# Kernel tuning notes

Hardware: AMD Instinct MI355X
Metric: run time of the kernel (lower is better)

## Reference

```python
import jax, jax.numpy as jnp
import numpy as np

N_NODES = 50000
N_GROUPS = 512
D_FEAT = 128
D_HID = 128
N_CLASS = 16
NEG_SLOPE = 0.2


def gat_conv(x, edge_index, W, a_src, a_dst, bias, n):
    """Single-head PyG-style GATConv (with self-loops, eval mode / no dropout)."""
    h = x @ W  # [n, D_HID]
    loop = jnp.arange(n)
    src = jnp.concatenate([edge_index[0], loop])  # neighbors j
    dst = jnp.concatenate([edge_index[1], loop])  # targets i
    a_s = h @ a_src  # [n]
    a_d = h @ a_dst  # [n]
    e = jax.nn.leaky_relu(a_s[src] + a_d[dst], NEG_SLOPE)  # [E+n]
    # segment softmax over incoming edges of each dst node
    m = jax.ops.segment_max(e, dst, num_segments=n)
    e = jnp.exp(e - m[dst])
    denom = jax.ops.segment_sum(e, dst, num_segments=n)
    alpha = e / denom[dst]
    out = jax.ops.segment_sum(alpha[:, None] * h[src], dst, num_segments=n)
    return out + bias


def setup_inputs() -> dict:
    key = jax.random.key(0)
    ks = jax.random.split(key, 12)
    s_f = 1.0 / np.sqrt(D_FEAT)
    s_h = 1.0 / np.sqrt(D_HID)
    return {
        "x_full": jax.random.normal(ks[0], (N_NODES, D_FEAT), jnp.float32),
        "x_group": jax.random.normal(ks[1], (N_GROUPS, D_FEAT), jnp.float32),
        "W_full": jax.random.normal(ks[2], (D_FEAT, D_HID), jnp.float32) * s_f,
        "a_src_full": jax.random.normal(ks[3], (D_HID,), jnp.float32) * s_h,
        "a_dst_full": jax.random.normal(ks[4], (D_HID,), jnp.float32) * s_h,
        "bias_full": jnp.zeros((D_HID,), jnp.float32),
        "W_group": jax.random.normal(ks[5], (D_FEAT, D_HID), jnp.float32) * s_f,
        "a_src_group": jax.random.normal(ks[6], (D_HID,), jnp.float32) * s_h,
        "a_dst_group": jax.random.normal(ks[7], (D_HID,), jnp.float32) * s_h,
        "bias_group": jnp.zeros((D_HID,), jnp.float32),
        "fc_W": jax.random.normal(ks[8], (D_HID, N_CLASS), jnp.float32) * s_h,
        "fc_b": jnp.zeros((N_CLASS,), jnp.float32),
        "edge_index_full": jax.random.randint(ks[9], (2, 600000), 0, N_NODES, jnp.int64),
        "edge_index_group": jax.random.randint(ks[10], (2, 4096), 0, N_GROUPS, jnp.int64),
        "node_group": jax.random.randint(ks[11], (N_NODES,), 0, N_GROUPS, jnp.int64),
    }


def reference(x_full, x_group, W_full, a_src_full, a_dst_full, bias_full,
              W_group, a_src_group, a_dst_group, bias_group, fc_W, fc_b,
              edge_index_full, edge_index_group, node_group):
    full_x = jax.nn.elu(gat_conv(x_full, edge_index_full, W_full, a_src_full,
                                 a_dst_full, bias_full, N_NODES))   # [N, D_HID]
    group_x = jax.nn.elu(gat_conv(x_group, edge_index_group, W_group, a_src_group,
                                  a_dst_group, bias_group, N_GROUPS))  # [G, D_HID]

    # mean feature of groups adjacent to each group (edges src->dst in group graph)
    gsrc, gdst = edge_index_group[0], edge_index_group[1]
    adj_sum = jax.ops.segment_sum(group_x[gdst], gsrc, num_segments=N_GROUPS)
    cnt = jax.ops.segment_sum(jnp.ones_like(gsrc, jnp.float32), gsrc, num_segments=N_GROUPS)
    adj_mean = adj_sum / jnp.maximum(cnt, 1.0)[:, None]  # [G, D_HID]

    gf = group_x[node_group]   # group feature per node, [N, D_HID]
    am = adj_mean[node_group]  # adjacent-group mean per node, [N, D_HID]

    # dot(node, group_feature) and mean_j dot(node, adj_j) == dot(node, adj_mean)
    iw_group = jnp.sum(full_x * gf, axis=-1, keepdims=True)  # [N, 1]
    iw_adj = jnp.sum(full_x * am, axis=-1, keepdims=True)    # [N, 1]

    updated = full_x + iw_group * gf + iw_adj * am  # [N, D_HID]
    out = updated @ fc_W + fc_b                     # [N, N_CLASS]
    return (out, updated)
```

## Files before the change

kernel.cpp:

```cpp
#include <hip/hip_runtime.h>

typedef unsigned short u16;
typedef unsigned int u32;

static __device__ __forceinline__ float lrelu(float x) { return x >= 0.f ? x : 0.2f * x; }

static __device__ __forceinline__ u16 f2bf(float f) {
    u32 u = __float_as_uint(f);
    u += 0x7FFF + ((u >> 16) & 1);
    return (u16)(u >> 16);
}
static __device__ __forceinline__ float bf2f(u16 h) {
    return __uint_as_float((u32)h << 16);
}

__global__ __launch_bounds__(256) void gemm_both_kernel(
        const float* __restrict__ Xf, const float* __restrict__ Wf,
        const float* __restrict__ asf, const float* __restrict__ adf,
        u16* __restrict__ Hbf, float* __restrict__ as_f, float* __restrict__ ad_f, int N,
        const float* __restrict__ Xg, const float* __restrict__ Wg,
        const float* __restrict__ asg, const float* __restrict__ adg,
        u16* __restrict__ Hbg, float* __restrict__ as_g, float* __restrict__ ad_g, int G,
        int nbFull) {
    const float* X; const float* W; const float* av; const float* dv;
    u16* Hb; float* as_out; float* ad_out; int n_lim; long base;
    if (blockIdx.x < nbFull) {
        X = Xf; W = Wf; av = asf; dv = adf; Hb = Hbf; as_out = as_f; ad_out = ad_f;
        n_lim = N; base = (long)blockIdx.x * 32;
    } else {
        X = Xg; W = Wg; av = asg; dv = adg; Hb = Hbg; as_out = as_g; ad_out = ad_g;
        n_lim = G; base = (long)(blockIdx.x - nbFull) * 32;
    }
    __shared__ float Ws[64 * 128];
    __shared__ float Xs[32 * 128];
    int tid = threadIdx.x;
    float4* Ws4 = (float4*)Ws;
    float4* Xs4 = (float4*)Xs;
    const float4* X4 = (const float4*)(X + base * 128);
    for (int i = tid; i < 1024; i += 256) {
        int r = i >> 5;
        Xs4[i] = (base + r < n_lim) ? X4[i] : make_float4(0.f, 0.f, 0.f, 0.f);
    }
    int fgrp = tid & 31;
    int n0 = (tid >> 5) * 4;
    float4 acc[4] = {};
    for (int half = 0; half < 2; ++half) {
        __syncthreads();
        const float4* W4 = (const float4*)(W + half * 64 * 128);
        for (int i = tid; i < 2048; i += 256) Ws4[i] = W4[i];
        __syncthreads();
        #pragma unroll 4
        for (int kk = 0; kk < 64; ++kk) {
            float4 w = Ws4[kk * 32 + fgrp];
            #pragma unroll
            for (int j = 0; j < 4; ++j) {
                float x = Xs[(n0 + j) * 128 + half * 64 + kk];
                acc[j].x += x * w.x; acc[j].y += x * w.y;
                acc[j].z += x * w.z; acc[j].w += x * w.w;
            }
        }
    }
    float4 as4 = ((const float4*)av)[fgrp];
    float4 ad4 = ((const float4*)dv)[fgrp];
    float ps[4], pd[4];
    #pragma unroll
    for (int j = 0; j < 4; ++j) {
        ps[j] = acc[j].x * as4.x + acc[j].y * as4.y + acc[j].z * as4.z + acc[j].w * as4.w;
        pd[j] = acc[j].x * ad4.x + acc[j].y * ad4.y + acc[j].z * ad4.z + acc[j].w * ad4.w;
    }
    #pragma unroll
    for (int off = 16; off; off >>= 1) {
        #pragma unroll
        for (int j = 0; j < 4; ++j) {
            ps[j] += __shfl_xor(ps[j], off);
            pd[j] += __shfl_xor(pd[j], off);
        }
    }
    if ((tid & 31) == 0) {
        #pragma unroll
        for (int j = 0; j < 4; ++j) {
            long n = base + n0 + j;
            if (n < n_lim) { as_out[n] = ps[j]; ad_out[n] = pd[j]; }
        }
    }
    #pragma unroll
    for (int j = 0; j < 4; ++j) {
        long n = base + n0 + j;
        if (n < n_lim) {
            ushort4 hv;
            hv.x = f2bf(acc[j].x); hv.y = f2bf(acc[j].y);
            hv.z = f2bf(acc[j].z); hv.w = f2bf(acc[j].w);
            ((ushort4*)(Hb + n * 128))[fgrp] = hv;
        }
    }
}

__global__ __launch_bounds__(256) void hist2_kernel(const int* __restrict__ efd, int E, int N,
                                                    const int* __restrict__ egd, int Eg, int G,
                                                    int Npad, int* __restrict__ deg) {
    int i = blockIdx.x * 256 + threadIdx.x;
    int totF = E + N;
    int tot = totF + Eg + G;
    if (i >= tot) return;
    int d;
    if (i < E) d = efd[i];
    else if (i < totF) d = i - E;
    else {
        int j = i - totF;
        d = Npad + ((j < Eg) ? egd[j] : (j - Eg));
    }
    atomicAdd(&deg[d], 1);
}

__global__ __launch_bounds__(256) void scan1_kernel(const int* __restrict__ deg, int n,
                                                    int* __restrict__ bsum) {
    __shared__ int s[256];
    int i = blockIdx.x * 256 + threadIdx.x;
    s[threadIdx.x] = (i < n) ? deg[i] : 0;
    __syncthreads();
    for (int off = 128; off; off >>= 1) {
        if (threadIdx.x < off) s[threadIdx.x] += s[threadIdx.x + off];
        __syncthreads();
    }
    if (threadIdx.x == 0) bsum[blockIdx.x] = s[0];
}

__global__ __launch_bounds__(256) void scan3_kernel(int* __restrict__ deg, int n, int nb,
                                                    const int* __restrict__ bsum,
                                                    int* __restrict__ offs, int Ltot) {
    __shared__ int sb[256];
    __shared__ int s[256];
    int t = threadIdx.x;
    sb[t] = (t < nb) ? bsum[t] : 0;
    __syncthreads();
    for (int off = 1; off < 256; off <<= 1) {
        int u = (t >= off) ? sb[t - off] : 0;
        __syncthreads();
        sb[t] += u;
        __syncthreads();
    }
    int blockOff = (blockIdx.x == 0) ? 0 : sb[blockIdx.x - 1];
    if (blockIdx.x == 0 && t == 0) offs[Ltot] = sb[nb - 1];

    int i = blockIdx.x * 256 + t;
    int v = (i < n) ? deg[i] : 0;
    s[t] = v;
    __syncthreads();
    for (int off = 1; off < 256; off <<= 1) {
        int u = (t >= off) ? s[t - off] : 0;
        __syncthreads();
        s[t] += u;
        __syncthreads();
    }
    if (i < n) {
        int excl = s[t] - v + blockOff;
        offs[i] = excl;
        deg[i] = excl;
    }
}

__global__ __launch_bounds__(256) void place2_kernel(const int* __restrict__ efs,
                                                     const int* __restrict__ efd, int E, int N,
                                                     const int* __restrict__ egs,
                                                     const int* __restrict__ egd, int Eg, int G,
                                                     int Npad,
                                                     const float* __restrict__ a_s,
                                                     const float* __restrict__ a_d,
                                                     const float* __restrict__ a_sg,
                                                     const float* __restrict__ a_dg,
                                                     int* __restrict__ cursor,
                                                     int* __restrict__ slot,
                                                     float* __restrict__ eslot) {
    int i = blockIdx.x * 256 + threadIdx.x;
    int totF = E + N;
    int tot = totF + Eg + G;
    if (i >= tot) return;
    int s, d, dcur;
    float av;
    if (i < totF) {
        if (i < E) { s = efs[i]; d = efd[i]; } else { s = d = i - E; }
        av = a_s[s] + a_d[d];
        dcur = d;
    } else {
        int j = i - totF;
        if (j < Eg) { s = egs[j]; d = egd[j]; } else { s = d = j - Eg; }
        av = a_sg[s] + a_dg[d];
        dcur = Npad + d;
    }
    float e = expf(lrelu(av));
    int pos = atomicAdd(&cursor[dcur], 1);
    slot[pos] = s;
    eslot[pos] = e;
}

__global__ __launch_bounds__(256) void pull2_kernel(const u16* __restrict__ Hf,
                                                    const u16* __restrict__ Hg,
                                                    const int* __restrict__ offs,
                                                    const int* __restrict__ slot,
                                                    const float* __restrict__ eslot,
                                                    const float* __restrict__ bias_f,
                                                    const float* __restrict__ bias_g,
                                                    float* __restrict__ fx,
                                                    float* __restrict__ gx,
                                                    int N, int G, int Npad) {
    int gid = blockIdx.x * 256 + threadIdx.x;
    int w = gid >> 6, lane = gid & 63;
    const u16* H;
    const float* bias;
    float* out;
    int idx;
    if (w < N) {
        H = Hf; bias = bias_f; out = fx + (long)w * 128; idx = w;
    } else if (w < N + G) {
        int g = w - N;
        H = Hg; bias = bias_g; out = gx + (long)g * 128; idx = Npad + g;
    } else return;
    int beg = offs[idx], end = offs[idx + 1];
    float accx = 0.f, accy = 0.f, ssum = 0.f;
    int k = beg;
    for (; k + 2 <= end; k += 2) {
        int s0 = slot[k], s1 = slot[k + 1];
        float e0 = eslot[k], e1 = eslot[k + 1];
        ushort2 h0 = ((const ushort2*)H)[(long)s0 * 64 + lane];
        ushort2 h1 = ((const ushort2*)H)[(long)s1 * 64 + lane];
        accx += e0 * bf2f(h0.x) + e1 * bf2f(h1.x);
        accy += e0 * bf2f(h0.y) + e1 * bf2f(h1.y);
        ssum += e0 + e1;
    }
    if (k < end) {
        int s0 = slot[k];
        float e0 = eslot[k];
        ushort2 h0 = ((const ushort2*)H)[(long)s0 * 64 + lane];
        accx += e0 * bf2f(h0.x);
        accy += e0 * bf2f(h0.y);
        ssum += e0;
    }
    float inv = 1.f / ssum;
    float2 b = ((const float2*)bias)[lane];
    float ox = accx * inv + b.x;
    float oy = accy * inv + b.y;
    ox = ox > 0.f ? ox : expm1f(ox);
    oy = oy > 0.f ? oy : expm1f(oy);
    ((float2*)out)[lane] = make_float2(ox, oy);
}

__global__ __launch_bounds__(256) void adj_kernel(const int* __restrict__ gsrc,
                                                  const int* __restrict__ gdst, int Eg,
                                                  const float* __restrict__ gx,
                                                  float* __restrict__ adj_sum,
                                                  float* __restrict__ cnt) {
    int gid = blockIdx.x * 256 + threadIdx.x;
    int i = gid >> 6, lane = gid & 63;
    if (i >= Eg) return;
    int s = gsrc[i], d = gdst[i];
    float2 gv = ((const float2*)gx)[(long)d * 64 + lane];
    atomicAdd(&adj_sum[(long)s * 128 + 2 * lane], gv.x);
    atomicAdd(&adj_sum[(long)s * 128 + 2 * lane + 1], gv.y);
    if (lane == 0) atomicAdd(&cnt[s], 1.f);
}

__global__ __launch_bounds__(256) void final_kernel(const int* __restrict__ node_group,
                                                    const float* __restrict__ gx,
                                                    const float* __restrict__ adj_sum,
                                                    const float* __restrict__ cnt,
                                                    const float* __restrict__ fcW,
                                                    const float* __restrict__ fcb,
                                                    float* __restrict__ upd,
                                                    float* __restrict__ out, int N) {
    int gid = blockIdx.x * 256 + threadIdx.x;
    int n = gid >> 6, lane = gid & 63;
    if (n >= N) return;
    int g = node_group[n];
    float2 row = ((const float2*)upd)[(long)n * 64 + lane];
    float2 gf = ((const float2*)gx)[(long)g * 64 + lane];
    float inv_cnt = 1.f / fmaxf(cnt[g], 1.f);
    float2 amv = ((const float2*)adj_sum)[(long)g * 64 + lane];
    float amx = amv.x * inv_cnt, amy = amv.y * inv_cnt;
    float pg = row.x * gf.x + row.y * gf.y;
    float pa = row.x * amx + row.y * amy;
    #pragma unroll
    for (int off = 32; off; off >>= 1) {
        pg += __shfl_xor(pg, off);
        pa += __shfl_xor(pa, off);
    }
    float ux = row.x + pg * gf.x + pa * amx;
    float uy = row.y + pg * gf.y + pa * amy;
    ((float2*)upd)[(long)n * 64 + lane] = make_float2(ux, uy);

    float v[16];
    const float4* fW4 = (const float4*)fcW;
    #pragma unroll
    for (int q = 0; q < 4; ++q) {
        float4 w0 = fW4[(2 * lane) * 4 + q];
        float4 w1 = fW4[(2 * lane + 1) * 4 + q];
        v[4 * q + 0] = ux * w0.x + uy * w1.x;
        v[4 * q + 1] = ux * w0.y + uy * w1.y;
        v[4 * q + 2] = ux * w0.z + uy * w1.z;
        v[4 * q + 3] = ux * w0.w + uy * w1.w;
    }
    #pragma unroll
    for (int stage = 0; stage < 4; ++stage) {
        int width = 32 >> stage;
        int half = 8 >> stage;
        bool hi = (lane & width) != 0;
        #pragma unroll
        for (int c = 0; c < half; ++c) {
            float send = hi ? v[c] : v[c + half];
            float recv = __shfl_xor(send, width);
            float keep = hi ? v[c + half] : v[c];
            v[c] = keep + recv;
        }
    }
    v[0] += __shfl_xor(v[0], 1);
    v[0] += __shfl_xor(v[0], 2);
    int cls = (lane >> 2) & 15;
    if ((lane & 3) == 0) out[(long)n * 16 + cls] = v[0] + fcb[cls];
}

extern "C" void kernel_launch(void* const* d_in, const int* in_sizes, int n_in,
                              void* d_out, int out_size, void* d_ws, size_t ws_size,
                              hipStream_t stream) {
    const float* x_full = (const float*)d_in[0];
    const float* x_group = (const float*)d_in[1];
    const float* W_full = (const float*)d_in[2];
    const float* a_src_full = (const float*)d_in[3];
    const float* a_dst_full = (const float*)d_in[4];
    const float* bias_full = (const float*)d_in[5];
    const float* W_group = (const float*)d_in[6];
    const float* a_src_g = (const float*)d_in[7];
    const float* a_dst_g = (const float*)d_in[8];
    const float* bias_g = (const float*)d_in[9];
    const float* fc_W = (const float*)d_in[10];
    const float* fc_b = (const float*)d_in[11];
    const int* ef = (const int*)d_in[12];
    const int* eg = (const int*)d_in[13];
    const int* node_group = (const int*)d_in[14];

    int N = in_sizes[0] / 128;
    int G = in_sizes[1] / 128;
    int E = in_sizes[12] / 2;
    int Eg = in_sizes[13] / 2;
    const int* ef_src = ef;
    const int* ef_dst = ef + E;
    const int* eg_src = eg;
    const int* eg_dst = eg + Eg;

    int Npad = (N + 255) & ~255;
    int Ltot = Npad + G;
    int LtotPad = (Ltot + 255) & ~255;
    int totF = E + N;
    int tot = totF + Eg + G;

    float* out_cls = (float*)d_out;
    float* fx = out_cls + (long)N * 16;

    char* w = (char*)d_ws;
    auto alloc = [&](size_t bytes) {
        char* p = w;
        w += (bytes + 255) & ~(size_t)255;
        return p;
    };
    u16* h_full = (u16*)alloc((size_t)N * 128 * 2);
    u16* h_g = (u16*)alloc((size_t)G * 128 * 2);
    float* a_s = (float*)alloc((size_t)N * 4);
    float* a_d = (float*)alloc((size_t)N * 4);
    float* a_sg = (float*)alloc((size_t)G * 4);
    float* a_dg = (float*)alloc((size_t)G * 4);
    float* gx = (float*)alloc((size_t)G * 128 * 4);
    float* adj_sum = (float*)alloc((size_t)G * 128 * 4);
    float* cnt = (float*)alloc((size_t)G * 4);
    int* deg = (int*)alloc((size_t)LtotPad * 4);
    int* offs = (int*)alloc((size_t)(LtotPad + 1) * 4);
    int* slot = (int*)alloc((size_t)tot * 4);
    float* eslot = (float*)alloc((size_t)tot * 4);
    int* bsum = (int*)alloc(256 * 4);

    size_t zero_span = (char*)(deg + LtotPad) - (char*)adj_sum;
    (void)hipMemsetAsync(adj_sum, 0, zero_span, stream);

    auto cdiv = [](int a, int b) { return (a + b - 1) / b; };

    int nbFull = cdiv(N, 32);
    gemm_both_kernel<<<nbFull + cdiv(G, 32), 256, 0, stream>>>(
        x_full, W_full, a_src_full, a_dst_full, h_full, a_s, a_d, N,
        x_group, W_group, a_src_g, a_dst_g, h_g, a_sg, a_dg, G, nbFull);

    int nb = cdiv(Ltot, 256);
    hist2_kernel<<<cdiv(tot, 256), 256, 0, stream>>>(ef_dst, E, N, eg_dst, Eg, G, Npad, deg);
    scan1_kernel<<<nb, 256, 0, stream>>>(deg, Ltot, bsum);
    scan3_kernel<<<nb, 256, 0, stream>>>(deg, Ltot, nb, bsum, offs, Ltot);
    place2_kernel<<<cdiv(tot, 256), 256, 0, stream>>>(ef_src, ef_dst, E, N, eg_src, eg_dst,
                                                      Eg, G, Npad, a_s, a_d, a_sg, a_dg,
                                                      deg, slot, eslot);

    pull2_kernel<<<cdiv((N + G) * 64, 256), 256, 0, stream>>>(h_full, h_g, offs, slot, eslot,
                                                              bias_full, bias_g, fx, gx,
                                                              N, G, Npad);

    adj_kernel<<<cdiv(Eg * 64, 256), 256, 0, stream>>>(eg_src, eg_dst, Eg, gx, adj_sum, cnt);
    final_kernel<<<cdiv(N * 64, 256), 256, 0, stream>>>(node_group, gx, adj_sum, cnt, fc_W,
                                                        fc_b, fx, out_cls, N);
}
```

Baseline: 337.7 us.

## Split final FC by linearity into per-node and per-group projections

Uses linearity of the classifier: out = full_x·W + pg·(gf·W) + pa·(am·W) + b. The full_x projection moves into the pull kernel's epilogue, and a new small kernel computes the per-group projections of group features and adjacent means. The final kernel then combines a few scalars per class instead of running the 16-wide shuffle reduction on every node. This adds a kernel launch, an N×16 intermediate buffer, and extra work and register pressure in the pull kernel.

```diff
diff --git a/kernel.cpp b/kernel.cpp
--- a/kernel.cpp
+++ b/kernel.cpp
@@ -12,6 +12,61 @@
 }
 static __device__ __forceinline__ float bf2f(u16 h) {
     return __uint_as_float((u32)h << 16);
+}
+
+static __device__ __forceinline__ float fc_reduce16(float f0, float f1, int lane,
+                                                    const float4* __restrict__ fW4) {
+    float4 w00 = fW4[(2 * lane) * 4 + 0], w01 = fW4[(2 * lane) * 4 + 1];
+    float4 w02 = fW4[(2 * lane) * 4 + 2], w03 = fW4[(2 * lane) * 4 + 3];
+    float4 w10 = fW4[(2 * lane + 1) * 4 + 0], w11 = fW4[(2 * lane + 1) * 4 + 1];
+    float4 w12 = fW4[(2 * lane + 1) * 4 + 2], w13 = fW4[(2 * lane + 1) * 4 + 3];
+    float4 q0, q1, q2, q3;
+    q0.x = f0 * w00.x + f1 * w10.x; q0.y = f0 * w00.y + f1 * w10.y;
+    q0.z = f0 * w00.z + f1 * w10.z; q0.w = f0 * w00.w + f1 * w10.w;
+    q1.x = f0 * w01.x + f1 * w11.x; q1.y = f0 * w01.y + f1 * w11.y;
+    q1.z = f0 * w01.z + f1 * w11.z; q1.w = f0 * w01.w + f1 * w11.w;
+    q2.x = f0 * w02.x + f1 * w12.x; q2.y = f0 * w02.y + f1 * w12.y;
+    q2.z = f0 * w02.z + f1 * w12.z; q2.w = f0 * w02.w + f1 * w12.w;
+    q3.x = f0 * w03.x + f1 * w13.x; q3.y = f0 * w03.y + f1 * w13.y;
+    q3.z = f0 * w03.z + f1 * w13.z; q3.w = f0 * w03.w + f1 * w13.w;
+    bool h5 = (lane & 32) != 0, h4 = (lane & 16) != 0;
+    bool h3 = (lane & 8) != 0, h2 = (lane & 4) != 0;
+    float4 s0, s1, k0, k1;
+    s0.x = h5 ? q0.x : q2.x; s0.y = h5 ? q0.y : q2.y;
+    s0.z = h5 ? q0.z : q2.z; s0.w = h5 ? q0.w : q2.w;
+    s1.x = h5 ? q1.x : q3.x; s1.y = h5 ? q1.y : q3.y;
+    s1.z = h5 ? q1.z : q3.z; s1.w = h5 ? q1.w : q3.w;
+    s0.x = __shfl_xor(s0.x, 32); s0.y = __shfl_xor(s0.y, 32);
+    s0.z = __shfl_xor(s0.z, 32); s0.w = __shfl_xor(s0.w, 32);
+    s1.x = __shfl_xor(s1.x, 32); s1.y = __shfl_xor(s1.y, 32);
+    s1.z = __shfl_xor(s1.z, 32); s1.w = __shfl_xor(s1.w, 32);
+    k0.x = h5 ? q2.x : q0.x; k0.y = h5 ? q2.y : q0.y;
+    k0.z = h5 ? q2.z : q0.z; k0.w = h5 ? q2.w : q0.w;
+    k1.x = h5 ? q3.x : q1.x; k1.y = h5 ? q3.y : q1.y;
+    k1.z = h5 ? q3.z : q1.z; k1.w = h5 ? q3.w : q1.w;
+    float4 a0, a1;
+    a0.x = k0.x + s0.x; a0.y = k0.y + s0.y; a0.z = k0.z + s0.z; a0.w = k0.w + s0.w;
+    a1.x = k1.x + s1.x; a1.y = k1.y + s1.y; a1.z = k1.z + s1.z; a1.w = k1.w + s1.w;
+    float4 sB, kB;
+    sB.x = h4 ? a0.x : a1.x; sB.y = h4 ? a0.y : a1.y;
+    sB.z = h4 ? a0.z : a1.z; sB.w = h4 ? a0.w : a1.w;
+    sB.x = __shfl_xor(sB.x, 16); sB.y = __shfl_xor(sB.y, 16);
+    sB.z = __shfl_xor(sB.z, 16); sB.w = __shfl_xor(sB.w, 16);
+    kB.x = h4 ? a1.x : a0.x; kB.y = h4 ? a1.y : a0.y;
+    kB.z = h4 ? a1.z : a0.z; kB.w = h4 ? a1.w : a0.w;
+    float4 b;
+    b.x = kB.x + sB.x; b.y = kB.y + sB.y; b.z = kB.z + sB.z; b.w = kB.w + sB.w;
+    float sCx = h3 ? b.x : b.z, sCy = h3 ? b.y : b.w;
+    sCx = __shfl_xor(sCx, 8); sCy = __shfl_xor(sCy, 8);
+    float kCx = h3 ? b.z : b.x, kCy = h3 ? b.w : b.y;
+    float c2x = kCx + sCx, c2y = kCy + sCy;
+    float sD = h2 ? c2x : c2y;
+    sD = __shfl_xor(sD, 4);
+    float kD = h2 ? c2y : c2x;
+    float r = kD + sD;
+    r += __shfl_xor(r, 1);
+    r += __shfl_xor(r, 2);
+    return r;
 }
 
 __global__ __launch_bounds__(256) void gemm_both_kernel(
@@ -200,8 +255,10 @@
                                                     const float* __restrict__ eslot,
                                                     const float* __restrict__ bias_f,
                                                     const float* __restrict__ bias_g,
+                                                    const float* __restrict__ fcW,
                                                     float* __restrict__ fx,
                                                     float* __restrict__ gx,
+                                                    float* __restrict__ fxW,
                                                     int N, int G, int Npad) {
     int gid = blockIdx.x * 256 + threadIdx.x;
     int w = gid >> 6, lane = gid & 63;
@@ -209,7 +266,8 @@
     const float* bias;
     float* out;
     int idx;
-    if (w < N) {
+    bool isFull = (w < N);
+    if (isFull) {
         H = Hf; bias = bias_f; out = fx + (long)w * 128; idx = w;
     } else if (w < N + G) {
         int g = w - N;
@@ -242,6 +300,11 @@
     ox = ox > 0.f ? ox : expm1f(ox);
     oy = oy > 0.f ? oy : expm1f(oy);
     ((float2*)out)[lane] = make_float2(ox, oy);
+    if (isFull) {
+        float r = fc_reduce16(ox, oy, lane, (const float4*)fcW);
+        int cls = (lane >> 2) & 15;
+        if ((lane & 3) == 0) fxW[(long)w * 16 + cls] = r;
+    }
 }
 
 __global__ __launch_bounds__(256) void adj_kernel(const int* __restrict__ gsrc,
@@ -259,62 +322,61 @@
     if (lane == 0) atomicAdd(&cnt[s], 1.f);
 }
 
-__global__ __launch_bounds__(256) void final_kernel(const int* __restrict__ node_group,
-                                                    const float* __restrict__ gx,
-                                                    const float* __restrict__ adj_sum,
-                                                    const float* __restrict__ cnt,
-                                                    const float* __restrict__ fcW,
-                                                    const float* __restrict__ fcb,
-                                                    float* __restrict__ upd,
-                                                    float* __restrict__ out, int N) {
+__global__ __launch_bounds__(256) void groupfc_kernel(const float* __restrict__ gx,
+                                                      const float* __restrict__ adj_sum,
+                                                      const float* __restrict__ cnt,
+                                                      const float* __restrict__ fcW,
+                                                      float* __restrict__ adj_mean,
+                                                      float* __restrict__ gfW,
+                                                      float* __restrict__ amW, int G) {
+    int gid = blockIdx.x * 256 + threadIdx.x;
+    int g = gid >> 6, lane = gid & 63;
+    if (g >= G) return;
+    float inv = 1.f / fmaxf(cnt[g], 1.f);
+    float2 as2 = ((const float2*)adj_sum)[(long)g * 64 + lane];
+    float2 am = make_float2(as2.x * inv, as2.y * inv);
+    ((float2*)adj_mean)[(long)g * 64 + lane] = am;
+    float2 gf = ((const float2*)gx)[(long)g * 64 + lane];
+    const float4* fW4 = (const float4*)fcW;
+    float rg = fc_reduce16(gf.x, gf.y, lane, fW4);
+    float ra = fc_reduce16(am.x, am.y, lane, fW4);
+    int cls = (lane >> 2) & 15;
+    if ((lane & 3) == 0) {
+        gfW[(long)g * 16 + cls] = rg;
+        amW[(long)g * 16 + cls] = ra;
+    }
+}
+
+__global__ __launch_bounds__(256) void final3_kernel(const int* __restrict__ node_group,
+                                                     const float* __restrict__ gx,
+                                                     const float* __restrict__ adj_mean,
+                                                     const float* __restrict__ gfW,
+                                                     const float* __restrict__ amW,
+                                                     const float* __restrict__ fxW,
+                                                     const float* __restrict__ fcb,
+                                                     float* __restrict__ upd,
+                                                     float* __restrict__ out, int N) {
     int gid = blockIdx.x * 256 + threadIdx.x;
     int n = gid >> 6, lane = gid & 63;
     if (n >= N) return;
     int g = node_group[n];
     float2 row = ((const float2*)upd)[(long)n * 64 + lane];
     float2 gf = ((const float2*)gx)[(long)g * 64 + lane];
-    float inv_cnt = 1.f / fmaxf(cnt[g], 1.f);
-    float2 amv = ((const float2*)adj_sum)[(long)g * 64 + lane];
-    float amx = amv.x * inv_cnt, amy = amv.y * inv_cnt;
+    float2 am = ((const float2*)adj_mean)[(long)g * 64 + lane];
     float pg = row.x * gf.x + row.y * gf.y;
-    float pa = row.x * amx + row.y * amy;
+    float pa = row.x * am.x + row.y * am.y;
     #pragma unroll
     for (int off = 32; off; off >>= 1) {
         pg += __shfl_xor(pg, off);
         pa += __shfl_xor(pa, off);
     }
-    float ux = row.x + pg * gf.x + pa * amx;
-    float uy = row.y + pg * gf.y + pa * amy;
+    float ux = row.x + pg * gf.x + pa * am.x;
+    float uy = row.y + pg * gf.y + pa * am.y;
     ((float2*)upd)[(long)n * 64 + lane] = make_float2(ux, uy);
-
-    float v[16];
-    const float4* fW4 = (const float4*)fcW;
-    #pragma unroll
-    for (int q = 0; q < 4; ++q) {
-        float4 w0 = fW4[(2 * lane) * 4 + q];
-        float4 w1 = fW4[(2 * lane + 1) * 4 + q];
-        v[4 * q + 0] = ux * w0.x + uy * w1.x;
-        v[4 * q + 1] = ux * w0.y + uy * w1.y;
-        v[4 * q + 2] = ux * w0.z + uy * w1.z;
-        v[4 * q + 3] = ux * w0.w + uy * w1.w;
-    }
-    #pragma unroll
-    for (int stage = 0; stage < 4; ++stage) {
-        int width = 32 >> stage;
-        int half = 8 >> stage;
-        bool hi = (lane & width) != 0;
-        #pragma unroll
-        for (int c = 0; c < half; ++c) {
-            float send = hi ? v[c] : v[c + half];
-            float recv = __shfl_xor(send, width);
-            float keep = hi ? v[c + half] : v[c];
-            v[c] = keep + recv;
-        }
-    }
-    v[0] += __shfl_xor(v[0], 1);
-    v[0] += __shfl_xor(v[0], 2);
-    int cls = (lane >> 2) & 15;
-    if ((lane & 3) == 0) out[(long)n * 16 + cls] = v[0] + fcb[cls];
+    if (lane < 16) {
+        out[(long)n * 16 + lane] = fxW[(long)n * 16 + lane] + pg * gfW[(long)g * 16 + lane] +
+                                   pa * amW[(long)g * 16 + lane] + fcb[lane];
+    }
 }
 
 extern "C" void kernel_launch(void* const* d_in, const int* in_sizes, int n_in,
@@ -367,6 +429,10 @@
     float* a_sg = (float*)alloc((size_t)G * 4);
     float* a_dg = (float*)alloc((size_t)G * 4);
     float* gx = (float*)alloc((size_t)G * 128 * 4);
+    float* adj_mean = (float*)alloc((size_t)G * 128 * 4);
+    float* fxW = (float*)alloc((size_t)N * 16 * 4);
+    float* gfW = (float*)alloc((size_t)G * 16 * 4);
+    float* amW = (float*)alloc((size_t)G * 16 * 4);
     float* adj_sum = (float*)alloc((size_t)G * 128 * 4);
     float* cnt = (float*)alloc((size_t)G * 4);
     int* deg = (int*)alloc((size_t)LtotPad * 4);
@@ -394,10 +460,12 @@
                                                       deg, slot, eslot);
 
     pull2_kernel<<<cdiv((N + G) * 64, 256), 256, 0, stream>>>(h_full, h_g, offs, slot, eslot,
-                                                              bias_full, bias_g, fx, gx,
-                                                              N, G, Npad);
+                                                              bias_full, bias_g, fc_W,
+                                                              fx, gx, fxW, N, G, Npad);
 
     adj_kernel<<<cdiv(Eg * 64, 256), 256, 0, stream>>>(eg_src, eg_dst, Eg, gx, adj_sum, cnt);
-    final_kernel<<<cdiv(N * 64, 256), 256, 0, stream>>>(node_group, gx, adj_sum, cnt, fc_W,
-                                                        fc_b, fx, out_cls, N);
-}
+    groupfc_kernel<<<cdiv(G * 64, 256), 256, 0, stream>>>(gx, adj_sum, cnt, fc_W,
+                                                          adj_mean, gfW, amW, G);
+    final3_kernel<<<cdiv(N * 64, 256), 256, 0, stream>>>(node_group, gx, adj_mean, gfW, amW,
+                                                         fxW, fc_b, fx, out_cls, N);
+}
```

Result: faster. 315.4 us (-6.6%).

## Fuse full-graph aggregation into final kernel, pack edge slots, widen gather loads

Applied to the files above, without the earlier changes.

Merges the degree histogram into the GEMM launch and splits the pull kernel. The group-graph aggregation now runs on its own first, and the full-graph aggregation is fused with the final interaction and classifier kernel, so the full_x intermediate is never written and re-read. Source index and edge weight are packed into one int2 array. The gather loads edge metadata cooperatively and broadcasts it with shuffles, with each wave processing four edges at once using 16-byte bf16 row loads. This adds register pressure and shuffle reductions, and wave utilisation drops for low-degree nodes because lanes are split into four sub-groups.

```diff
diff --git a/kernel.cpp b/kernel.cpp
--- a/kernel.cpp
+++ b/kernel.cpp
@@ -10,18 +10,37 @@
     u += 0x7FFF + ((u >> 16) & 1);
     return (u16)(u >> 16);
 }
-static __device__ __forceinline__ float bf2f(u16 h) {
-    return __uint_as_float((u32)h << 16);
-}
-
-__global__ __launch_bounds__(256) void gemm_both_kernel(
+static __device__ __forceinline__ float bflo(u32 u) { return __uint_as_float(u << 16); }
+static __device__ __forceinline__ float bfhi(u32 u) { return __uint_as_float(u & 0xffff0000u); }
+
+__global__ __launch_bounds__(256) void gemm_hist_kernel(
         const float* __restrict__ Xf, const float* __restrict__ Wf,
         const float* __restrict__ asf, const float* __restrict__ adf,
         u16* __restrict__ Hbf, float* __restrict__ as_f, float* __restrict__ ad_f, int N,
         const float* __restrict__ Xg, const float* __restrict__ Wg,
         const float* __restrict__ asg, const float* __restrict__ adg,
         u16* __restrict__ Hbg, float* __restrict__ as_g, float* __restrict__ ad_g, int G,
-        int nbFull) {
+        int nbFull, int nbGemm,
+        const int* __restrict__ efd, int E, const int* __restrict__ egd, int Eg,
+        int Npad, int* __restrict__ deg) {
+    __shared__ float Ws[64 * 128];
+    __shared__ float Xs[32 * 128];
+    int tid = threadIdx.x;
+    if (blockIdx.x >= nbGemm) {
+        int i = (blockIdx.x - nbGemm) * 256 + tid;
+        int totF = E + N;
+        int tot = totF + Eg + G;
+        if (i >= tot) return;
+        int d;
+        if (i < E) d = efd[i];
+        else if (i < totF) d = i - E;
+        else {
+            int j = i - totF;
+            d = Npad + ((j < Eg) ? egd[j] : (j - Eg));
+        }
+        atomicAdd(&deg[d], 1);
+        return;
+    }
     const float* X; const float* W; const float* av; const float* dv;
     u16* Hb; float* as_out; float* ad_out; int n_lim; long base;
     if (blockIdx.x < nbFull) {
@@ -31,9 +50,6 @@
         X = Xg; W = Wg; av = asg; dv = adg; Hb = Hbg; as_out = as_g; ad_out = ad_g;
         n_lim = G; base = (long)(blockIdx.x - nbFull) * 32;
     }
-    __shared__ float Ws[64 * 128];
-    __shared__ float Xs[32 * 128];
-    int tid = threadIdx.x;
     float4* Ws4 = (float4*)Ws;
     float4* Xs4 = (float4*)Xs;
     const float4* X4 = (const float4*)(X + base * 128);
@@ -95,23 +111,6 @@
     }
 }
 
-__global__ __launch_bounds__(256) void hist2_kernel(const int* __restrict__ efd, int E, int N,
-                                                    const int* __restrict__ egd, int Eg, int G,
-                                                    int Npad, int* __restrict__ deg) {
-    int i = blockIdx.x * 256 + threadIdx.x;
-    int totF = E + N;
-    int tot = totF + Eg + G;
-    if (i >= tot) return;
-    int d;
-    if (i < E) d = efd[i];
-    else if (i < totF) d = i - E;
-    else {
-        int j = i - totF;
-        d = Npad + ((j < Eg) ? egd[j] : (j - Eg));
-    }
-    atomicAdd(&deg[d], 1);
-}
-
 __global__ __launch_bounds__(256) void scan1_kernel(const int* __restrict__ deg, int n,
                                                     int* __restrict__ bsum) {
     __shared__ int s[256];
@@ -169,8 +168,7 @@
                                                      const float* __restrict__ a_sg,
                                                      const float* __restrict__ a_dg,
                                                      int* __restrict__ cursor,
-                                                     int* __restrict__ slot,
-                                                     float* __restrict__ eslot) {
+                                                     int2* __restrict__ sepack) {
     int i = blockIdx.x * 256 + threadIdx.x;
     int totF = E + N;
     int tot = totF + Eg + G;
@@ -189,59 +187,121 @@
     }
     float e = expf(lrelu(av));
     int pos = atomicAdd(&cursor[dcur], 1);
-    slot[pos] = s;
-    eslot[pos] = e;
-}
-
-__global__ __launch_bounds__(256) void pull2_kernel(const u16* __restrict__ Hf,
-                                                    const u16* __restrict__ Hg,
-                                                    const int* __restrict__ offs,
-                                                    const int* __restrict__ slot,
-                                                    const float* __restrict__ eslot,
-                                                    const float* __restrict__ bias_f,
-                                                    const float* __restrict__ bias_g,
-                                                    float* __restrict__ fx,
-                                                    float* __restrict__ gx,
-                                                    int N, int G, int Npad) {
+    sepack[pos] = make_int2(s, __float_as_int(e));
+}
+
+#define PULL_GATHER_BODY(H16, beg, end)                                          \
+    for (int b = (beg); b < (end); b += 64) {                                    \
+        int m = (end) - b;                                                       \
+        if (m > 64) m = 64;                                                      \
+        int2 se = (lane < m) ? sepack[b + lane] : make_int2(0, 0);               \
+        int sl = se.x;                                                           \
+        float el = __int_as_float(se.y);                                         \
+        int kend = (m + 3) & ~3;                                                 \
+        int k = 0;                                                               \
+        for (; k + 16 <= kend; k += 16) {                                        \
+            int s0 = __shfl(sl, k + sub);                                        \
+            float e0 = __shfl(el, k + sub);                                      \
+            int s1 = __shfl(sl, k + 4 + sub);                                    \
+            float e1 = __shfl(el, k + 4 + sub);                                  \
+            int s2 = __shfl(sl, k + 8 + sub);                                    \
+            float e2 = __shfl(el, k + 8 + sub);                                  \
+            int s3 = __shfl(sl, k + 12 + sub);                                   \
+            float e3 = __shfl(el, k + 12 + sub);                                 \
+            uint4 h0 = H16[(long)s0 * 16 + fc];                                  \
+            uint4 h1 = H16[(long)s1 * 16 + fc];                                  \
+            uint4 h2 = H16[(long)s2 * 16 + fc];                                  \
+            uint4 h3 = H16[(long)s3 * 16 + fc];                                  \
+            a0 += e0 * bflo(h0.x); a1 += e0 * bfhi(h0.x);                        \
+            a2 += e0 * bflo(h0.y); a3 += e0 * bfhi(h0.y);                        \
+            a4 += e0 * bflo(h0.z); a5 += e0 * bfhi(h0.z);                        \
+            a6 += e0 * bflo(h0.w); a7 += e0 * bfhi(h0.w);                        \
+            a0 += e1 * bflo(h1.x); a1 += e1 * bfhi(h1.x);                        \
+            a2 += e1 * bflo(h1.y); a3 += e1 * bfhi(h1.y);                        \
+            a4 += e1 * bflo(h1.z); a5 += e1 * bfhi(h1.z);                        \
+            a6 += e1 * bflo(h1.w); a7 += e1 * bfhi(h1.w);                        \
+            a0 += e2 * bflo(h2.x); a1 += e2 * bfhi(h2.x);                        \
+            a2 += e2 * bflo(h2.y); a3 += e2 * bfhi(h2.y);                        \
+            a4 += e2 * bflo(h2.z); a5 += e2 * bfhi(h2.z);                        \
+            a6 += e2 * bflo(h2.w); a7 += e2 * bfhi(h2.w);                        \
+            a0 += e3 * bflo(h3.x); a1 += e3 * bfhi(h3.x);                        \
+            a2 += e3 * bflo(h3.y); a3 += e3 * bfhi(h3.y);                        \
+            a4 += e3 * bflo(h3.z); a5 += e3 * bfhi(h3.z);                        \
+            a6 += e3 * bflo(h3.w); a7 += e3 * bfhi(h3.w);                        \
+            ss += (e0 + e1) + (e2 + e3);                                         \
+        }                                                                        \
+        for (; k + 8 <= kend; k += 8) {                                          \
+            int s0 = __shfl(sl, k + sub);                                        \
+            float e0 = __shfl(el, k + sub);                                      \
+            int s1 = __shfl(sl, k + 4 + sub);                                    \
+            float e1 = __shfl(el, k + 4 + sub);                                  \
+            uint4 h0 = H16[(long)s0 * 16 + fc];                                  \
+            uint4 h1 = H16[(long)s1 * 16 + fc];                                  \
+            a0 += e0 * bflo(h0.x); a1 += e0 * bfhi(h0.x);                        \
+            a2 += e0 * bflo(h0.y); a3 += e0 * bfhi(h0.y);                        \
+            a4 += e0 * bflo(h0.z); a5 += e0 * bfhi(h0.z);                        \
+            a6 += e0 * bflo(h0.w); a7 += e0 * bfhi(h0.w);                        \
+            a0 += e1 * bflo(h1.x); a1 += e1 * bfhi(h1.x);                        \
+            a2 += e1 * bflo(h1.y); a3 += e1 * bfhi(h1.y);                        \
+            a4 += e1 * bflo(h1.z); a5 += e1 * bfhi(h1.z);                        \
+            a6 += e1 * bflo(h1.w); a7 += e1 * bfhi(h1.w);                        \
+            ss += e0 + e1;                                                       \
+        }                                                                        \
+        if (k < kend) {                                                          \
+            int s0 = __shfl(sl, k + sub);                                        \
+            float e0 = __shfl(el, k + sub);                                      \
+            uint4 h0 = H16[(long)s0 * 16 + fc];                                  \
+            a0 += e0 * bflo(h0.x); a1 += e0 * bfhi(h0.x);                        \
+            a2 += e0 * bflo(h0.y); a3 += e0 * bfhi(h0.y);                        \
+            a4 += e0 * bflo(h0.z); a5 += e0 * bfhi(h0.z);                        \
+            a6 += e0 * bflo(h0.w); a7 += e0 * bfhi(h0.w);                        \
+            ss += e0;                                                            \
+        }                                                                        \
+    }                                                                            \
+    a0 += __shfl_xor(a0, 16); a0 += __shfl_xor(a0, 32);                          \
+    a1 += __shfl_xor(a1, 16); a1 += __shfl_xor(a1, 32);                          \
+    a2 += __shfl_xor(a2, 16); a2 += __shfl_xor(a2, 32);                          \
+    a3 += __shfl_xor(a3, 16); a3 += __shfl_xor(a3, 32);                          \
+    a4 += __shfl_xor(a4, 16); a4 += __shfl_xor(a4, 32);                          \
+    a5 += __shfl_xor(a5, 16); a5 += __shfl_xor(a5, 32);                          \
+    a6 += __shfl_xor(a6, 16); a6 += __shfl_xor(a6, 32);                          \
+    a7 += __shfl_xor(a7, 16); a7 += __shfl_xor(a7, 32);                          \
+    ss += __shfl_xor(ss, 16); ss += __shfl_xor(ss, 32);
+
+__global__ __launch_bounds__(256) void pull_g_kernel(const u16* __restrict__ Hg,
+                                                     const int* __restrict__ offs,
+                                                     const int2* __restrict__ sepack,
+                                                     const float* __restrict__ bias_g,
+                                                     float* __restrict__ gx,
+                                                     int G, int Npad) {
     int gid = blockIdx.x * 256 + threadIdx.x;
     int w = gid >> 6, lane = gid & 63;
-    const u16* H;
-    const float* bias;
-    float* out;
-    int idx;
-    if (w < N) {
-        H = Hf; bias = bias_f; out = fx + (long)w * 128; idx = w;
-    } else if (w < N + G) {
-        int g = w - N;
-        H = Hg; bias = bias_g; out = gx + (long)g * 128; idx = Npad + g;
-    } else return;
+    if (w >= G) return;
+    int idx = Npad + w;
     int beg = offs[idx], end = offs[idx + 1];
-    float accx = 0.f, accy = 0.f, ssum = 0.f;
-    int k = beg;
-    for (; k + 2 <= end; k += 2) {
-        int s0 = slot[k], s1 = slot[k + 1];
-        float e0 = eslot[k], e1 = eslot[k + 1];
-        ushort2 h0 = ((const ushort2*)H)[(long)s0 * 64 + lane];
-        ushort2 h1 = ((const ushort2*)H)[(long)s1 * 64 + lane];
-        accx += e0 * bf2f(h0.x) + e1 * bf2f(h1.x);
-        accy += e0 * bf2f(h0.y) + e1 * bf2f(h1.y);
-        ssum += e0 + e1;
-    }
-    if (k < end) {
-        int s0 = slot[k];
-        float e0 = eslot[k];
-        ushort2 h0 = ((const ushort2*)H)[(long)s0 * 64 + lane];
-        accx += e0 * bf2f(h0.x);
-        accy += e0 * bf2f(h0.y);
-        ssum += e0;
-    }
-    float inv = 1.f / ssum;
-    float2 b = ((const float2*)bias)[lane];
-    float ox = accx * inv + b.x;
-    float oy = accy * inv + b.y;
-    ox = ox > 0.f ? ox : expm1f(ox);
-    oy = oy > 0.f ? oy : expm1f(oy);
-    ((float2*)out)[lane] = make_float2(ox, oy);
+    const uint4* H16 = (const uint4*)Hg;
+    int sub = lane >> 4;
+    int fc = lane & 15;
+    float a0 = 0.f, a1 = 0.f, a2 = 0.f, a3 = 0.f;
+    float a4 = 0.f, a5 = 0.f, a6 = 0.f, a7 = 0.f;
+    float ss = 0.f;
+    PULL_GATHER_BODY(H16, beg, end)
+    if (sub == 0) {
+        float inv = 1.f / ss;
+        const float4* b4 = (const float4*)bias_g;
+        float4 bA = b4[fc * 2], bB = b4[fc * 2 + 1];
+        float o0 = a0 * inv + bA.x, o1 = a1 * inv + bA.y;
+        float o2 = a2 * inv + bA.z, o3 = a3 * inv + bA.w;
+        float o4 = a4 * inv + bB.x, o5 = a5 * inv + bB.y;
+        float o6 = a6 * inv + bB.z, o7 = a7 * inv + bB.w;
+        o0 = o0 > 0.f ? o0 : expm1f(o0); o1 = o1 > 0.f ? o1 : expm1f(o1);
+        o2 = o2 > 0.f ? o2 : expm1f(o2); o3 = o3 > 0.f ? o3 : expm1f(o3);
+        o4 = o4 > 0.f ? o4 : expm1f(o4); o5 = o5 > 0.f ? o5 : expm1f(o5);
+        o6 = o6 > 0.f ? o6 : expm1f(o6); o7 = o7 > 0.f ? o7 : expm1f(o7);
+        float4* o4p = (float4*)(gx + (long)w * 128);
+        o4p[fc * 2] = make_float4(o0, o1, o2, o3);
+        o4p[fc * 2 + 1] = make_float4(o4, o5, o6, o7);
+    }
 }
 
 __global__ __launch_bounds__(256) void adj_kernel(const int* __restrict__ gsrc,
@@ -259,62 +319,96 @@
     if (lane == 0) atomicAdd(&cnt[s], 1.f);
 }
 
-__global__ __launch_bounds__(256) void final_kernel(const int* __restrict__ node_group,
-                                                    const float* __restrict__ gx,
-                                                    const float* __restrict__ adj_sum,
-                                                    const float* __restrict__ cnt,
-                                                    const float* __restrict__ fcW,
-                                                    const float* __restrict__ fcb,
-                                                    float* __restrict__ upd,
-                                                    float* __restrict__ out, int N) {
+__global__ __launch_bounds__(256) void pull_f_final_kernel(
+        const u16* __restrict__ Hf,
+        const int* __restrict__ offs,
+        const int2* __restrict__ sepack,
+        const float* __restrict__ bias_f,
+        const int* __restrict__ node_group,
+        const float* __restrict__ gx,
+        const float* __restrict__ adj_sum,
+        const float* __restrict__ cnt,
+        const float* __restrict__ fcW,
+        const float* __restrict__ fcb,
+        float* __restrict__ upd,
+        float* __restrict__ out, int N) {
     int gid = blockIdx.x * 256 + threadIdx.x;
-    int n = gid >> 6, lane = gid & 63;
-    if (n >= N) return;
-    int g = node_group[n];
-    float2 row = ((const float2*)upd)[(long)n * 64 + lane];
-    float2 gf = ((const float2*)gx)[(long)g * 64 + lane];
+    int w = gid >> 6, lane = gid & 63;
+    if (w >= N) return;
+    int beg = offs[w], end = offs[w + 1];
+    const uint4* H16 = (const uint4*)Hf;
+    int sub = lane >> 4;
+    int fc = lane & 15;
+    float a0 = 0.f, a1 = 0.f, a2 = 0.f, a3 = 0.f;
+    float a4 = 0.f, a5 = 0.f, a6 = 0.f, a7 = 0.f;
+    float ss = 0.f;
+    PULL_GATHER_BODY(H16, beg, end)
+    float inv = 1.f / ss;
+    const float4* b4 = (const float4*)bias_f;
+    float4 bA = b4[fc * 2], bB = b4[fc * 2 + 1];
+    float o0 = a0 * inv + bA.x, o1 = a1 * inv + bA.y;
+    float o2 = a2 * inv + bA.z, o3 = a3 * inv + bA.w;
+    float o4 = a4 * inv + bB.x, o5 = a5 * inv + bB.y;
+    float o6 = a6 * inv + bB.z, o7 = a7 * inv + bB.w;
+    o0 = o0 > 0.f ? o0 : expm1f(o0); o1 = o1 > 0.f ? o1 : expm1f(o1);
+    o2 = o2 > 0.f ? o2 : expm1f(o2); o3 = o3 > 0.f ? o3 : expm1f(o3);
+    o4 = o4 > 0.f ? o4 : expm1f(o4); o5 = o5 > 0.f ? o5 : expm1f(o5);
+    o6 = o6 > 0.f ? o6 : expm1f(o6); o7 = o7 > 0.f ? o7 : expm1f(o7);
+    int g = node_group[w];
+    const float4* gx4 = (const float4*)(gx + (long)g * 128);
+    const float4* am4 = (const float4*)(adj_sum + (long)g * 128);
     float inv_cnt = 1.f / fmaxf(cnt[g], 1.f);
-    float2 amv = ((const float2*)adj_sum)[(long)g * 64 + lane];
-    float amx = amv.x * inv_cnt, amy = amv.y * inv_cnt;
-    float pg = row.x * gf.x + row.y * gf.y;
-    float pa = row.x * amx + row.y * amy;
+    float4 gfA = gx4[fc * 2], gfB = gx4[fc * 2 + 1];
+    float4 amA = am4[fc * 2], amB = am4[fc * 2 + 1];
+    amA.x *= inv_cnt; amA.y *= inv_cnt; amA.z *= inv_cnt; amA.w *= inv_cnt;
+    amB.x *= inv_cnt; amB.y *= inv_cnt; amB.z *= inv_cnt; amB.w *= inv_cnt;
+    float pg = o0 * gfA.x + o1 * gfA.y + o2 * gfA.z + o3 * gfA.w +
+               o4 * gfB.x + o5 * gfB.y + o6 * gfB.z + o7 * gfB.w;
+    float pa = o0 * amA.x + o1 * amA.y + o2 * amA.z + o3 * amA.w +
+               o4 * amB.x + o5 * amB.y + o6 * amB.z + o7 * amB.w;
     #pragma unroll
-    for (int off = 32; off; off >>= 1) {
-        pg += __shfl_xor(pg, off);
-        pa += __shfl_xor(pa, off);
-    }
-    float ux = row.x + pg * gf.x + pa * amx;
-    float uy = row.y + pg * gf.y + pa * amy;
-    ((float2*)upd)[(long)n * 64 + lane] = make_float2(ux, uy);
-
-    float v[16];
+    for (int mask = 8; mask; mask >>= 1) {
+        pg += __shfl_xor(pg, mask);
+        pa += __shfl_xor(pa, mask);
+    }
+    float u0 = o0 + pg * gfA.x + pa * amA.x;
+    float u1 = o1 + pg * gfA.y + pa * amA.y;
+    float u2 = o2 + pg * gfA.z + pa * amA.z;
+    float u3 = o3 + pg * gfA.w + pa * amA.w;
+    float u4 = o4 + pg * gfB.x + pa * amB.x;
+    float u5 = o5 + pg * gfB.y + pa * amB.y;
+    float u6 = o6 + pg * gfB.z + pa * amB.z;
+    float u7 = o7 + pg * gfB.w + pa * amB.w;
+    if (sub == 0) {
+        float4* o4p = (float4*)(upd + (long)w * 128);
+        o4p[fc * 2] = make_float4(u0, u1, u2, u3);
+        o4p[fc * 2 + 1] = make_float4(u4, u5, u6, u7);
+    }
     const float4* fW4 = (const float4*)fcW;
+    int rb = (8 * fc) * 4 + sub;
+    float4 w0 = fW4[rb], w1 = fW4[rb + 4], w2 = fW4[rb + 8], w3 = fW4[rb + 12];
+    float4 w4 = fW4[rb + 16], w5 = fW4[rb + 20], w6 = fW4[rb + 24], w7 = fW4[rb + 28];
+    float4 p;
+    p.x = u0 * w0.x + u1 * w1.x + u2 * w2.x + u3 * w3.x +
+          u4 * w4.x + u5 * w5.x + u6 * w6.x + u7 * w7.x;
+    p.y = u0 * w0.y + u1 * w1.y + u2 * w2.y + u3 * w3.y +
+          u4 * w4.y + u5 * w5.y + u6 * w6.y + u7 * w7.y;
+    p.z = u0 * w0.z + u1 * w1.z + u2 * w2.z + u3 * w3.z +
+          u4 * w4.z + u5 * w5.z + u6 * w6.z + u7 * w7.z;
+    p.w = u0 * w0.w + u1 * w1.w + u2 * w2.w + u3 * w3.w +
+          u4 * w4.w + u5 * w5.w + u6 * w6.w + u7 * w7.w;
     #pragma unroll
-    for (int q = 0; q < 4; ++q) {
-        float4 w0 = fW4[(2 * lane) * 4 + q];
-        float4 w1 = fW4[(2 * lane + 1) * 4 + q];
-        v[4 * q + 0] = ux * w0.x + uy * w1.x;
-        v[4 * q + 1] = ux * w0.y + uy * w1.y;
-        v[4 * q + 2] = ux * w0.z + uy * w1.z;
-        v[4 * q + 3] = ux * w0.w + uy * w1.w;
-    }
-    #pragma unroll
-    for (int stage = 0; stage < 4; ++stage) {
-        int width = 32 >> stage;
-        int half = 8 >> stage;
-        bool hi = (lane & width) != 0;
-        #pragma unroll
-        for (int c = 0; c < half; ++c) {
-            float send = hi ? v[c] : v[c + half];
-            float recv = __shfl_xor(send, width);
-            float keep = hi ? v[c + half] : v[c];
-            v[c] = keep + recv;
-        }
-    }
-    v[0] += __shfl_xor(v[0], 1);
-    v[0] += __shfl_xor(v[0], 2);
-    int cls = (lane >> 2) & 15;
-    if ((lane & 3) == 0) out[(long)n * 16 + cls] = v[0] + fcb[cls];
+    for (int mask = 8; mask; mask >>= 1) {
+        p.x += __shfl_xor(p.x, mask);
+        p.y += __shfl_xor(p.y, mask);
+        p.z += __shfl_xor(p.z, mask);
+        p.w += __shfl_xor(p.w, mask);
+    }
+    if (fc == 0) {
+        float4 bb = ((const float4*)fcb)[sub];
+        p.x += bb.x; p.y += bb.y; p.z += bb.z; p.w += bb.w;
+        ((float4*)(out + (long)w * 16))[sub] = p;
+    }
 }
 
 extern "C" void kernel_launch(void* const* d_in, const int* in_sizes, int n_in,
@@ -352,7 +446,7 @@
     int tot = totF + Eg + G;
 
     float* out_cls = (float*)d_out;
-    float* fx = out_cls + (long)N * 16;
+    float* upd = out_cls + (long)N * 16;
 
     char* w = (char*)d_ws;
     auto alloc = [&](size_t bytes) {
@@ -371,8 +465,7 @@
     float* cnt = (float*)alloc((size_t)G * 4);
     int* deg = (int*)alloc((size_t)LtotPad * 4);
     int* offs = (int*)alloc((size_t)(LtotPad + 1) * 4);
-    int* slot = (int*)alloc((size_t)tot * 4);
-    float* eslot = (float*)alloc((size_t)tot * 4);
+    int2* sepack = (int2*)alloc((size_t)tot * 8);
     int* bsum = (int*)alloc(256 * 4);
 
     size_t zero_span = (char*)(deg + LtotPad) - (char*)adj_sum;
@@ -381,23 +474,24 @@
     auto cdiv = [](int a, int b) { return (a + b - 1) / b; };
 
     int nbFull = cdiv(N, 32);
-    gemm_both_kernel<<<nbFull + cdiv(G, 32), 256, 0, stream>>>(
+    int nbGemm = nbFull + cdiv(G, 32);
+    int nbHist = cdiv(tot, 256);
+    gemm_hist_kernel<<<nbGemm + nbHist, 256, 0, stream>>>(
         x_full, W_full, a_src_full, a_dst_full, h_full, a_s, a_d, N,
-        x_group, W_group, a_src_g, a_dst_g, h_g, a_sg, a_dg, G, nbFull);
+        x_group, W_group, a_src_g, a_dst_g, h_g, a_sg, a_dg, G,
+        nbFull, nbGemm, ef_dst, E, eg_dst, Eg, Npad, deg);
 
     int nb = cdiv(Ltot, 256);
-    hist2_kernel<<<cdiv(tot, 256), 256, 0, stream>>>(ef_dst, E, N, eg_dst, Eg, G, Npad, deg);
     scan1_kernel<<<nb, 256, 0, stream>>>(deg, Ltot, bsum);
     scan3_kernel<<<nb, 256, 0, stream>>>(deg, Ltot, nb, bsum, offs, Ltot);
     place2_kernel<<<cdiv(tot, 256), 256, 0, stream>>>(ef_src, ef_dst, E, N, eg_src, eg_dst,
                                                       Eg, G, Npad, a_s, a_d, a_sg, a_dg,
-                                                      deg, slot, eslot);
-
-    pull2_kernel<<<cdiv((N + G) * 64, 256), 256, 0, stream>>>(h_full, h_g, offs, slot, eslot,
-                                                              bias_full, bias_g, fx, gx,
-                                                              N, G, Npad);
-
+                                                      deg, sepack);
+
+    pull_g_kernel<<<cdiv(G * 64, 256), 256, 0, stream>>>(h_g, offs, sepack, bias_g,
+                                                         gx, G, Npad);
     adj_kernel<<<cdiv(Eg * 64, 256), 256, 0, stream>>>(eg_src, eg_dst, Eg, gx, adj_sum, cnt);
-    final_kernel<<<cdiv(N * 64, 256), 256, 0, stream>>>(node_group, gx, adj_sum, cnt, fc_W,
-                                                        fc_b, fx, out_cls, N);
-}
+    pull_f_final_kernel<<<cdiv(N * 64, 256), 256, 0, stream>>>(
+        h_full, offs, sepack, bias_full, node_group, gx, adj_sum, cnt,
+        fc_W, fc_b, upd, out_cls, N);
+}
```

Measured after the change: 274.4 us. 18.7% less time.
